# Kernel tuning notes

Measured on AMD Instinct MI355X. Metric: run time of the kernel, lower is better.

Reference implementation:

```python
import jax, jax.numpy as jnp
import numpy as np

B, T, F_IN = 64, 396, 128
D_MODEL, N_HEAD, D_QKV, D_FF = 768, 8, 96, 3072
N_LAYERS, N_OUT, REL_D = 6, 256, 100


def setup_inputs():
    key = jax.random.key(0)
    cnt = [0]
    def rn(shape, std=1.0):
        cnt[0] += 1
        return jax.random.normal(jax.random.fold_in(key, cnt[0]), shape, jnp.float32) * std
    inp = {"x_raw": rn((B, T, F_IN))}
    def add_rb(p, cin, cout):
        inp[p + "_c1_w"] = rn((cout, cin, 3), (2.0 / (cin * 3)) ** 0.5)
        inp[p + "_c1_b"] = rn((cout,), 0.01)
        inp[p + "_bn1_s"] = 1.0 + rn((cout,), 0.1)
        inp[p + "_bn1_b"] = rn((cout,), 0.1)
        inp[p + "_c2_w"] = rn((cout, cout, 3), (2.0 / (cout * 3)) ** 0.5)
        inp[p + "_c2_b"] = rn((cout,), 0.01)
        inp[p + "_bn2_s"] = 1.0 + rn((cout,), 0.1)
        inp[p + "_bn2_b"] = rn((cout,), 0.1)
        inp[p + "_cr_w"] = rn((cout, cin, 1), (2.0 / cin) ** 0.5)
        inp[p + "_cr_b"] = rn((cout,), 0.01)
        inp[p + "_bnr_s"] = 1.0 + rn((cout,), 0.1)
        inp[p + "_bnr_b"] = rn((cout,), 0.1)
    add_rb("rb1", F_IN, D_MODEL)
    add_rb("rb2", D_MODEL, D_MODEL)
    inp["w_in_w"] = rn((D_MODEL, D_MODEL), D_MODEL ** -0.5)
    inp["w_in_b"] = rn((D_MODEL,), 0.01)
    inp["cls_token"] = jnp.zeros((1, 1, D_MODEL), jnp.float32)
    xav = (2.0 / (D_MODEL + D_QKV)) ** 0.5
    inp["wq"] = rn((N_LAYERS, N_HEAD, D_MODEL, D_QKV), xav)
    inp["wk"] = rn((N_LAYERS, N_HEAD, D_MODEL, D_QKV), xav)
    inp["wv"] = rn((N_LAYERS, N_HEAD, D_MODEL, D_QKV), xav)
    inp["wo"] = rn((N_LAYERS, N_HEAD, D_QKV, D_MODEL), xav)
    inp["rel_emb"] = rn((N_LAYERS, N_HEAD, 2 * REL_D + 1, D_QKV), D_QKV ** -0.5)
    inp["ln1_g"] = jnp.ones((N_LAYERS, D_MODEL), jnp.float32)
    inp["ln1_b"] = jnp.zeros((N_LAYERS, D_MODEL), jnp.float32)
    inp["ln2_g"] = jnp.ones((N_LAYERS, D_MODEL), jnp.float32)
    inp["ln2_b"] = jnp.zeros((N_LAYERS, D_MODEL), jnp.float32)
    inp["ff1_w"] = rn((N_LAYERS, D_FF, D_MODEL), (2.0 / D_MODEL) ** 0.5)
    inp["ff1_b"] = rn((N_LAYERS, D_FF), 0.01)
    inp["ff2_w"] = rn((N_LAYERS, D_MODEL, D_FF), (1.0 / D_FF) ** 0.5)
    inp["ff2_b"] = rn((N_LAYERS, D_MODEL), 0.01)
    inp["w_out_w"] = rn((N_OUT, D_MODEL), D_MODEL ** -0.5)
    inp["w_out_b"] = rn((N_OUT,), 0.01)
    return inp


def _conv1d(x, w, b, stride=1):
    # x: [B, Cin, T], w: [Cout, Cin, K]
    pad = (w.shape[-1] - 1) // 2
    y = jax.lax.conv_general_dilated(x, w, (stride,), [(pad, pad)],
                                     dimension_numbers=("NCH", "OIH", "NCH"))
    return y + b[None, :, None]


def _bn(x, s, b):
    # eval-mode BatchNorm1d folded into per-channel affine
    return x * s[None, :, None] + b[None, :, None]


def _resblock(x, c1w, c1b, s1, b1, c2w, c2b, s2, b2, crw, crb, sr, br, stride):
    h = jax.nn.relu(_bn(_conv1d(x, c1w, c1b, stride), s1, b1))
    h = _bn(_conv1d(h, c2w, c2b), s2, b2)
    r = _bn(_conv1d(x, crw, crb, stride), sr, br)
    return jax.nn.relu(h + r)


def _layer_norm(x, g, b, eps=1e-5):
    m = jnp.mean(x, -1, keepdims=True)
    v = jnp.mean((x - m) ** 2, -1, keepdims=True)
    return (x - m) * jax.lax.rsqrt(v + eps) * g + b


def _attention(x, wq, wk, wv, wo, rel):
    # x: [B, L, D]; relative-positional attention (fairseq LearnedRelativePositionalEmbedding, unmasked)
    L = x.shape[1]
    q = jnp.einsum("btf,hfa->bhta", x, wq) * (D_QKV ** -0.5)
    k = jnp.einsum("btf,hfa->bhta", x, wk)
    v = jnp.einsum("btf,hfa->bhta", x, wv)
    logits = jnp.einsum("bhqa,bhka->bhqk", q, k)
    # narrow embeddings to the 2L-1 relative positions used (L <= REL_D)
    start = REL_D - L
    rel_used = rel[:, start:start + 2 * L - 1, :]  # [h, 2L-1, a]
    pos_all = jnp.einsum("bhqa,hma->bhqm", q, rel_used)  # [B,h,L,2L-1]
    idx = jnp.arange(L)[None, :] - jnp.arange(L)[:, None] + (L - 1)  # [L,L], rel->abs skew
    logits = logits + jnp.take_along_axis(pos_all, idx[None, None], axis=3)
    probs = jax.nn.softmax(logits, axis=-1)
    o = jnp.einsum("bhqk,bhka->bhqa", probs, v)
    return jnp.einsum("bhta,haf->btf", o, wo)


def reference(x_raw, rb1_c1_w, rb1_c1_b, rb1_bn1_s, rb1_bn1_b, rb1_c2_w, rb1_c2_b, rb1_bn2_s, rb1_bn2_b, rb1_cr_w, rb1_cr_b, rb1_bnr_s, rb1_bnr_b, rb2_c1_w, rb2_c1_b, rb2_bn1_s, rb2_bn1_b, rb2_c2_w, rb2_c2_b, rb2_bn2_s, rb2_bn2_b, rb2_cr_w, rb2_cr_b, rb2_bnr_s, rb2_bnr_b, w_in_w, w_in_b, cls_token, wq, wk, wv, wo, rel_emb, ln1_g, ln1_b, ln2_g, ln2_b, ff1_w, ff1_b, ff2_w, ff2_b, w_out_w, w_out_b):
    x = jnp.transpose(x_raw, (0, 2, 1))  # [B, F_IN, T]
    x = _resblock(x, rb1_c1_w, rb1_c1_b, rb1_bn1_s, rb1_bn1_b, rb1_c2_w, rb1_c2_b, rb1_bn2_s, rb1_bn2_b, rb1_cr_w, rb1_cr_b, rb1_bnr_s, rb1_bnr_b, 2)
    x = _resblock(x, rb2_c1_w, rb2_c1_b, rb2_bn1_s, rb2_bn1_b, rb2_c2_w, rb2_c2_b, rb2_bn2_s, rb2_bn2_b, rb2_cr_w, rb2_cr_b, rb2_bnr_s, rb2_bnr_b, 2)
    x = jnp.transpose(x, (0, 2, 1))  # [B, T', D]
    x = x @ w_in_w.T + w_in_b
    cls = jnp.broadcast_to(cls_token, (x.shape[0], 1, D_MODEL))
    x = jnp.concatenate([cls, x], axis=1)  # [B, L, D], L = T'+1
    for l in range(N_LAYERS):
        a = _attention(x, wq[l], wk[l], wv[l], wo[l], rel_emb[l])
        x = _layer_norm(x + a, ln1_g[l], ln1_b[l])
        h = jax.nn.relu(x @ ff1_w[l].T + ff1_b[l]) @ ff2_w[l].T + ff2_b[l]
        x = _layer_norm(x + h, ln2_g[l], ln2_b[l])
    return x[:, 0, :] @ w_out_w.T + w_out_b
```

## Files before the change

kernel.cpp:

```cpp
#include <hip/hip_runtime.h>

typedef _Float16 h8 __attribute__((ext_vector_type(8)));
typedef float f4 __attribute__((ext_vector_type(4)));

namespace {

constexpr int DM   = 768;
constexpr int NHEAD= 8;
constexpr int DQ   = 96;
constexpr int DFF  = 3072;
constexpr int NL   = 6;
constexpr int B_   = 64;
constexpr int T0   = 396, T1 = 198, T2 = 99;
constexpr int FIN  = 128;
constexpr int L_   = 100;
constexpr int MSEQ = B_ * L_;
constexpr int M1   = B_ * T1;
constexpr int M2   = B_ * T2;
constexpr int NREL = 201;
constexpr int POSN = 256;
constexpr int RELK = 128;

enum { EPI_F32 = 0, EPI_RELU_H, EPI_H, EPI_CONV_F32, EPI_CONV_RELU_H, EPI_CONV_ADD_RELU_H };

__device__ __forceinline__ void g2l16(const _Float16* g, _Float16* l)
{
    __builtin_amdgcn_global_load_lds(
        (const __attribute__((address_space(1))) unsigned int*)g,
        (__attribute__((address_space(3))) unsigned int*)l,
        16, 0, 0);
}

template<bool CONV, int EPI, bool OPAD, int MI>
__global__ __launch_bounds__(256)
void gemm6_k(const _Float16* __restrict__ A, const _Float16* __restrict__ B,
             float* __restrict__ Cf, _Float16* __restrict__ Ch,
             const float* __restrict__ bias, const float* __restrict__ bns,
             const float* __restrict__ bnb, const float* __restrict__ res,
             int M, int N, int K, int lda,
             int T_out, int Tp_in, int stride_t, int KS, int in_off,
             int gx, int gxy,
             size_t a_z, size_t b_z, size_t c_z)
{
    constexpr int TM = MI * 32;
    __shared__ _Float16 As[2][TM * 64];
    __shared__ _Float16 Bs[2][128 * 64];

    const unsigned nwg = gridDim.x, orig = blockIdx.x;
    const unsigned q = nwg >> 3, rr_ = nwg & 7;
    const unsigned xcd = orig & 7, idx = orig >> 3;
    const unsigned wgid = (xcd < rr_) ? xcd * (q + 1) + idx
                                      : rr_ * (q + 1) + (xcd - rr_) * q + idx;
    const int bz  = (int)(wgid / (unsigned)gxy);
    const int rem = (int)(wgid - (unsigned)bz * (unsigned)gxy);
    const int by  = rem / gx;
    const int bx  = rem - by * gx;

    A += (size_t)bz * a_z;
    B += (size_t)bz * b_z;

    const int tid  = threadIdx.x;
    const int lane = tid & 63;
    const int wid  = tid >> 6;
    const int m0   = by * TM;
    const int n0   = bx * 128;
    const int wm   = (wid >> 1) * (MI * 16);
    const int wn   = (wid & 1) * 64;

    f4 acc[MI][4];
    #pragma unroll
    for (int i = 0; i < MI; ++i)
        #pragma unroll
        for (int j = 0; j < 4; ++j)
            #pragma unroll
            for (int p = 0; p < 4; ++p) acc[i][j][p] = 0.0f;

    const int colh = (((lane & 7) ^ ((lane >> 3) & 7)) << 3);
    size_t aoff[MI];
    #pragma unroll
    for (int i = 0; i < MI; ++i) {
        int m = min(m0 + wid * (MI * 8) + i * 8 + (lane >> 3), M - 1);
        if (CONV) {
            int ab = m / T_out, at = m - ab * T_out;
            aoff[i] = ((size_t)ab * Tp_in + at * stride_t + in_off) * lda + colh;
        } else {
            aoff[i] = (size_t)m * lda + colh;
        }
    }
    size_t boff[4];
    #pragma unroll
    for (int i = 0; i < 4; ++i)
        boff[i] = (size_t)(n0 + wid * 32 + i * 8 + (lane >> 3)) * K + colh;
    const size_t bdk = (size_t)N * K;

    const int fr  = lane & 15;
    const int grp = lane >> 4;

    const int ks64 = K >> 6;
    const int NS   = (CONV ? KS : 1) * ks64;

    auto stage = [&](int step, int buf) {
        int dk = 0, kk = step;
        if (CONV) { dk = step / ks64; kk = step - dk * ks64; }
        const int k0  = kk << 6;
        const size_t adk = CONV ? (size_t)dk * lda : 0;
        const size_t bdo = (size_t)dk * bdk;
        #pragma unroll
        for (int i = 0; i < MI; ++i)
            g2l16(A + aoff[i] + adk + k0, &As[buf][(wid * (MI * 8) + i * 8) * 64]);
        #pragma unroll
        for (int i = 0; i < 4; ++i)
            g2l16(B + boff[i] + bdo + k0, &Bs[buf][(wid * 32 + i * 8) * 64]);
    };

    stage(0, 0);
    __syncthreads();

    for (int step = 0; step < NS; ++step) {
        const int cur = step & 1;
        const _Float16* As_ = As[cur];
        const _Float16* Bs_ = Bs[cur];

        const int co0 = ((grp ^ (fr & 7)) << 3);
        h8 af0[MI], bf0[4];
        #pragma unroll
        for (int mi = 0; mi < MI; ++mi)
            af0[mi] = *(const h8*)&As_[(wm + mi * 16 + fr) * 64 + co0];
        #pragma unroll
        for (int ni = 0; ni < 4; ++ni)
            bf0[ni] = *(const h8*)&Bs_[(wn + ni * 16 + fr) * 64 + co0];

        if (step + 1 < NS) stage(step + 1, cur ^ 1);

        #pragma unroll
        for (int mi = 0; mi < MI; ++mi)
            #pragma unroll
            for (int ni = 0; ni < 4; ++ni)
                acc[mi][ni] = __builtin_amdgcn_mfma_f32_16x16x32_f16(
                    af0[mi], bf0[ni], acc[mi][ni], 0, 0, 0);

        const int co1 = (((4 + grp) ^ (fr & 7)) << 3);
        h8 af1[MI], bf1[4];
        #pragma unroll
        for (int mi = 0; mi < MI; ++mi)
            af1[mi] = *(const h8*)&As_[(wm + mi * 16 + fr) * 64 + co1];
        #pragma unroll
        for (int ni = 0; ni < 4; ++ni)
            bf1[ni] = *(const h8*)&Bs_[(wn + ni * 16 + fr) * 64 + co1];
        #pragma unroll
        for (int mi = 0; mi < MI; ++mi)
            #pragma unroll
            for (int ni = 0; ni < 4; ++ni)
                acc[mi][ni] = __builtin_amdgcn_mfma_f32_16x16x32_f16(
                    af1[mi], bf1[ni], acc[mi][ni], 0, 0, 0);

        __syncthreads();
    }

    const int frc = lane & 15;
    const int fq4 = (lane >> 4) * 4;
    float*    Cfo = Cf ? Cf + (size_t)bz * c_z : nullptr;
    _Float16* Cho = Ch ? Ch + (size_t)bz * c_z : nullptr;
    #pragma unroll
    for (int mi = 0; mi < MI; ++mi)
        #pragma unroll
        for (int ni = 0; ni < 4; ++ni)
            #pragma unroll
            for (int r = 0; r < 4; ++r) {
                int row = m0 + wm + mi * 16 + fq4 + r;
                int col = n0 + wn + ni * 16 + frc;
                if (row >= M) continue;
                float v = acc[mi][ni][r];
                size_t roff;
                if (OPAD) {
                    int ab = row / T_out, at = row - ab * T_out;
                    roff = ((size_t)ab * (T_out + 2) + at + 1) * N + col;
                } else {
                    roff = (size_t)row * N + col;
                }
                if (EPI == EPI_F32) {
                    if (bias) v += bias[col];
                    Cfo[roff] = v;
                } else if (EPI == EPI_RELU_H) {
                    if (bias) v += bias[col];
                    Cho[roff] = (_Float16)fmaxf(v, 0.0f);
                } else if (EPI == EPI_H) {
                    Cho[roff] = (_Float16)v;
                } else if (EPI == EPI_CONV_F32) {
                    v = bns[col] * (v + bias[col]) + bnb[col];
                    Cfo[roff] = v;
                } else if (EPI == EPI_CONV_RELU_H) {
                    v = bns[col] * (v + bias[col]) + bnb[col];
                    Cho[roff] = (_Float16)fmaxf(v, 0.0f);
                } else {
                    v = bns[col] * (v + bias[col]) + bnb[col] + res[(size_t)row * N + col];
                    Cho[roff] = (_Float16)fmaxf(v, 0.0f);
                }
            }
}


__global__ void f2h_k(const float* __restrict__ in, _Float16* __restrict__ out,
                      long n, float scale)
{
    long i = (long)blockIdx.x * blockDim.x + threadIdx.x;
    if (i < n) out[i] = (_Float16)(in[i] * scale);
}

__global__ void f2h_pad_k(const float* __restrict__ in, _Float16* __restrict__ out)
{
    long i = (long)blockIdx.x * blockDim.x + threadIdx.x;
    if (i >= (long)B_ * 398 * FIN) return;
    int  c = (int)(i % FIN);
    long r = i / FIN;
    int  t = (int)(r % 398);
    int  b = (int)(r / 398);
    float v = (t == 0 || t == 397) ? 0.0f
            : in[((long)b * T0 + (t - 1)) * FIN + c];
    out[i] = (_Float16)v;
}

__global__ void zero_pad_k(_Float16* __restrict__ buf, int Tp, int C)
{
    long i = (long)blockIdx.x * blockDim.x + threadIdx.x;
    if (i >= (long)B_ * 2 * C) return;
    int  c = (int)(i % C);
    long r = i / C;
    int  hi = (int)(r % 2);
    int  b  = (int)(r / 2);
    buf[((size_t)b * Tp + (hi ? Tp - 1 : 0)) * C + c] = (_Float16)0.0f;
}

__global__ void pack_qkv_k(const float* __restrict__ wq, const float* __restrict__ wk,
                           const float* __restrict__ wv, _Float16* __restrict__ out)
{
    long i = (long)blockIdx.x * blockDim.x + threadIdx.x;
    if (i >= (long)NL * 2304 * DM) return;
    int  f = (int)(i % DM);
    long r = i / DM;
    int  n = (int)(r % 2304);
    int  l = (int)(r / 2304);
    int  s = n / DM, hn = n % DM, h = hn / DQ, a = hn % DQ;
    const float* src = (s == 0) ? wq : ((s == 1) ? wk : wv);
    out[i] = (_Float16)src[(((long)l * NHEAD + h) * DM + f) * DQ + a];
}

__global__ void pack_wo_k(const float* __restrict__ wo, _Float16* __restrict__ out)
{
    long i = (long)blockIdx.x * blockDim.x + threadIdx.x;
    if (i >= (long)NL * DM * DM) return;
    int  ha = (int)(i % DM);
    long r  = i / DM;
    int  f  = (int)(r % DM);
    int  l  = (int)(r / DM);
    int  h = ha / DQ, a = ha % DQ;
    out[i] = (_Float16)wo[(((long)l * NHEAD + h) * DQ + a) * DM + f];
}

__global__ void pack_conv_k(const float* __restrict__ w, _Float16* __restrict__ out,
                            int Cout, int Cin, int KS)
{
    long i = (long)blockIdx.x * blockDim.x + threadIdx.x;
    if (i >= (long)Cout * Cin * KS) return;
    int  ci = (int)(i % Cin);
    long r  = i / Cin;
    int  co = (int)(r % Cout);
    int  dk = (int)(r / Cout);
    out[i] = (_Float16)w[((long)co * Cin + ci) * KS + dk];
}

__global__ void pack_rel_k(const float* __restrict__ rel, _Float16* __restrict__ out)
{
    long i = (long)blockIdx.x * blockDim.x + threadIdx.x;
    if (i >= (long)NL * NHEAD * POSN * RELK) return;
    int  k = (int)(i & (RELK - 1));
    long r = i >> 7;
    int  n = (int)(r & (POSN - 1));
    long r2 = r >> 8;
    int  h = (int)(r2 & (NHEAD - 1));
    int  l = (int)(r2 >> 3);
    float v = 0.0f;
    if (n < NREL && k < DQ)
        v = rel[(((long)l * NHEAD + h) * NREL + n) * DQ + k] * 0.10206207261596575f;
    out[i] = (_Float16)v;
}

__global__ void concat_k(const float* __restrict__ xlin, const float* __restrict__ cls,
                         float* __restrict__ xf, _Float16* __restrict__ xh)
{
    long i = (long)blockIdx.x * blockDim.x + threadIdx.x;
    if (i >= (long)MSEQ * DM) return;
    int  c = (int)(i % DM);
    long m = i / DM;
    int  b = (int)(m / L_), t = (int)(m % L_);
    float v = (t == 0) ? cls[c] : xlin[((long)b * (L_ - 1) + (t - 1)) * DM + c];
    xf[i] = v;
    xh[i] = (_Float16)v;
}

__global__ __launch_bounds__(256)
void ln_k(const float* x, const float* __restrict__ d,
          const float* __restrict__ g, const float* __restrict__ bb,
          float* xo, _Float16* __restrict__ xh)
{
    long row = blockIdx.x;
    const float* xr = x + row * DM;
    const float* dr = d + row * DM;
    float v[3];
    float s = 0.0f;
    #pragma unroll
    for (int k = 0; k < 3; ++k) {
        int c = threadIdx.x + 256 * k;
        v[k] = xr[c] + dr[c];
        s += v[k];
    }
    __shared__ float red[8];
    #pragma unroll
    for (int o = 32; o; o >>= 1) s += __shfl_xor(s, o, 64);
    int w = threadIdx.x >> 6, lane = threadIdx.x & 63;
    if (lane == 0) red[w] = s;
    __syncthreads();
    s = red[0] + red[1] + red[2] + red[3];
    float mean = s * (1.0f / DM);
    float vs = 0.0f;
    #pragma unroll
    for (int k = 0; k < 3; ++k) { float t = v[k] - mean; vs += t * t; }
    #pragma unroll
    for (int o = 32; o; o >>= 1) vs += __shfl_xor(vs, o, 64);
    if (lane == 0) red[4 + w] = vs;
    __syncthreads();
    vs = red[4] + red[5] + red[6] + red[7];
    float rstd = rsqrtf(vs * (1.0f / DM) + 1e-5f);
    #pragma unroll
    for (int k = 0; k < 3; ++k) {
        int c = threadIdx.x + 256 * k;
        float y = (v[k] - mean) * rstd * g[c] + bb[c];
        xo[row * DM + c] = y;
        xh[row * DM + c] = (_Float16)y;
    }
}

constexpr int LP = 128;
constexpr int KP = 104;
constexpr int PP = 136;

__global__ __launch_bounds__(256)
void attn_k(const _Float16* __restrict__ qkv, const _Float16* __restrict__ pos,
            _Float16* __restrict__ o)
{
    __shared__ __align__(16) char smem[60928];
    _Float16* Ks = (_Float16*)smem;
    _Float16* Ps = (_Float16*)smem;
    _Float16* Vt = (_Float16*)(smem + 34816);

    const int h = blockIdx.x, b = blockIdx.y;
    const int tid = threadIdx.x, lane = tid & 63, w = tid >> 6;
    const _Float16* base = qkv + (size_t)b * L_ * 2304 + h * DQ;
    const float qscale = 0.10206207261596575f;

    {
        int row = tid >> 1;
        int c0  = (tid & 1) * 48;
        const bool real = row < L_;
        const _Float16* krow = base + 768 + (size_t)row * 2304;
        #pragma unroll
        for (int q = 0; q < 6; ++q) {
            int c = c0 + q * 8;
            h8 kv;
            #pragma unroll
            for (int e = 0; e < 8; ++e) kv[e] = (_Float16)0.0f;
            if (real) kv = *(const h8*)(krow + c);
            *(h8*)&Ks[row * KP + c] = kv;
        }
        for (int idx = tid; idx < DQ * LP; idx += 256) {
            int a = idx % DQ, j = idx / DQ;
            _Float16 v = (_Float16)0.0f;
            if (j < L_) v = base[1536 + (size_t)j * 2304 + a];
            Vt[a * PP + j] = v;
        }
    }
    __syncthreads();

    const int fr = lane & 15;
    const int fk = (lane >> 4) * 8;
    const int rbase = w * 32 + ((lane >> 4) << 2);

    f4 acc[2][8];
    #pragma unroll
    for (int mi = 0; mi < 2; ++mi)
        #pragma unroll
        for (int ni = 0; ni < 8; ++ni)
            #pragma unroll
            for (int q = 0; q < 4; ++q) acc[mi][ni][q] = 0.0f;

    #pragma unroll
    for (int k0 = 0; k0 < DQ; k0 += 32) {
        h8 a0 = *(const h8*)(base + (size_t)(w * 32 + fr) * 2304 + k0 + fk);
        h8 a1 = *(const h8*)(base + (size_t)(w * 32 + 16 + fr) * 2304 + k0 + fk);
        #pragma unroll
        for (int ni = 0; ni < 8; ++ni) {
            h8 bv = *(const h8*)&Ks[(ni * 16 + fr) * KP + k0 + fk];
            acc[0][ni] = __builtin_amdgcn_mfma_f32_16x16x32_f16(a0, bv, acc[0][ni], 0, 0, 0);
            acc[1][ni] = __builtin_amdgcn_mfma_f32_16x16x32_f16(a1, bv, acc[1][ni], 0, 0, 0);
        }
    }

    const _Float16* posb = pos + ((size_t)h * MSEQ + (size_t)b * L_) * POSN;
    #pragma unroll
    for (int mi = 0; mi < 2; ++mi)
        #pragma unroll
        for (int r = 0; r < 4; ++r) {
            int i = rbase + mi * 16 + r;
            float s[8];
            #pragma unroll
            for (int ni = 0; ni < 8; ++ni) {
                int j = ni * 16 + fr;
                float v = -3.0e38f;
                if (i < L_ && j < L_)
                    v = acc[mi][ni][r] * qscale
                      + (float)posb[(size_t)i * POSN + (j - i + (L_ - 1))];
                s[ni] = v;
            }
            float m = s[0];
            #pragma unroll
            for (int ni = 1; ni < 8; ++ni) m = fmaxf(m, s[ni]);
            #pragma unroll
            for (int msk = 1; msk < 16; msk <<= 1) m = fmaxf(m, __shfl_xor(m, msk, 64));
            float sum = 0.0f;
            #pragma unroll
            for (int ni = 0; ni < 8; ++ni) { s[ni] = __expf(s[ni] - m); sum += s[ni]; }
            #pragma unroll
            for (int msk = 1; msk < 16; msk <<= 1) sum += __shfl_xor(sum, msk, 64);
            float inv = 1.0f / sum;
            #pragma unroll
            for (int ni = 0; ni < 8; ++ni) acc[mi][ni][r] = s[ni] * inv;
        }

    __syncthreads();

    #pragma unroll
    for (int mi = 0; mi < 2; ++mi)
        #pragma unroll
        for (int r = 0; r < 4; ++r) {
            int i = rbase + mi * 16 + r;
            #pragma unroll
            for (int ni = 0; ni < 8; ++ni)
                Ps[i * PP + ni * 16 + fr] = (_Float16)acc[mi][ni][r];
        }
    __syncthreads();

    f4 acc2[2][6];
    #pragma unroll
    for (int mi = 0; mi < 2; ++mi)
        #pragma unroll
        for (int ni = 0; ni < 6; ++ni)
            #pragma unroll
            for (int q = 0; q < 4; ++q) acc2[mi][ni][q] = 0.0f;

    #pragma unroll
    for (int k0 = 0; k0 < LP; k0 += 32) {
        h8 a0 = *(const h8*)&Ps[(w * 32 + fr) * PP + k0 + fk];
        h8 a1 = *(const h8*)&Ps[(w * 32 + 16 + fr) * PP + k0 + fk];
        #pragma unroll
        for (int ni = 0; ni < 6; ++ni) {
            h8 bv = *(const h8*)&Vt[(ni * 16 + fr) * PP + k0 + fk];
            acc2[0][ni] = __builtin_amdgcn_mfma_f32_16x16x32_f16(a0, bv, acc2[0][ni], 0, 0, 0);
            acc2[1][ni] = __builtin_amdgcn_mfma_f32_16x16x32_f16(a1, bv, acc2[1][ni], 0, 0, 0);
        }
    }

    _Float16* ob = o + (size_t)b * L_ * DM + h * DQ;
    #pragma unroll
    for (int mi = 0; mi < 2; ++mi)
        #pragma unroll
        for (int r = 0; r < 4; ++r) {
            int i = rbase + mi * 16 + r;
            if (i < L_) {
                #pragma unroll
                for (int ni = 0; ni < 6; ++ni)
                    ob[(size_t)i * DM + ni * 16 + fr] = (_Float16)acc2[mi][ni][r];
            }
        }
}

__global__ __launch_bounds__(256)
void out_k(const float* __restrict__ xseq, const float* __restrict__ w,
           const float* __restrict__ bias, float* __restrict__ out)
{
    __shared__ float xs[DM];
    int b = blockIdx.x;
    for (int c = threadIdx.x; c < DM; c += 256) xs[c] = xseq[(size_t)b * L_ * DM + c];
    __syncthreads();
    int n = threadIdx.x;
    const f4* wr = (const f4*)(w + (size_t)n * DM);
    float acc = 0.0f;
    #pragma unroll 4
    for (int k4 = 0; k4 < DM / 4; ++k4) {
        f4 wv = wr[k4];
        f4 xv = *(const f4*)&xs[k4 * 4];
        acc += wv[0]*xv[0] + wv[1]*xv[1] + wv[2]*xv[2] + wv[3]*xv[3];
    }
    out[(size_t)b * 256 + n] = acc + bias[n];
}

}

extern "C" void kernel_launch(void* const* d_in, const int* in_sizes, int n_in,
                              void* d_out, int out_size, void* d_ws, size_t ws_size,
                              hipStream_t stream)
{
    (void)in_sizes; (void)n_in; (void)out_size; (void)ws_size;

    const float* x_raw   = (const float*)d_in[0];
    const float* rb1_c1w = (const float*)d_in[1];
    const float* rb1_c1b = (const float*)d_in[2];
    const float* rb1_s1  = (const float*)d_in[3];
    const float* rb1_b1  = (const float*)d_in[4];
    const float* rb1_c2w = (const float*)d_in[5];
    const float* rb1_c2b = (const float*)d_in[6];
    const float* rb1_s2  = (const float*)d_in[7];
    const float* rb1_b2  = (const float*)d_in[8];
    const float* rb1_crw = (const float*)d_in[9];
    const float* rb1_crb = (const float*)d_in[10];
    const float* rb1_sr  = (const float*)d_in[11];
    const float* rb1_br  = (const float*)d_in[12];
    const float* rb2_c1w = (const float*)d_in[13];
    const float* rb2_c1b = (const float*)d_in[14];
    const float* rb2_s1  = (const float*)d_in[15];
    const float* rb2_b1  = (const float*)d_in[16];
    const float* rb2_c2w = (const float*)d_in[17];
    const float* rb2_c2b = (const float*)d_in[18];
    const float* rb2_s2  = (const float*)d_in[19];
    const float* rb2_b2  = (const float*)d_in[20];
    const float* rb2_crw = (const float*)d_in[21];
    const float* rb2_crb = (const float*)d_in[22];
    const float* rb2_sr  = (const float*)d_in[23];
    const float* rb2_br  = (const float*)d_in[24];
    const float* w_in_w  = (const float*)d_in[25];
    const float* w_in_b  = (const float*)d_in[26];
    const float* cls     = (const float*)d_in[27];
    const float* wq      = (const float*)d_in[28];
    const float* wk      = (const float*)d_in[29];
    const float* wv      = (const float*)d_in[30];
    const float* wo      = (const float*)d_in[31];
    const float* rel     = (const float*)d_in[32];
    const float* ln1g    = (const float*)d_in[33];
    const float* ln1b    = (const float*)d_in[34];
    const float* ln2g    = (const float*)d_in[35];
    const float* ln2b    = (const float*)d_in[36];
    const float* ff1w    = (const float*)d_in[37];
    const float* ff1b    = (const float*)d_in[38];
    const float* ff2w    = (const float*)d_in[39];
    const float* ff2b    = (const float*)d_in[40];
    const float* w_out_w = (const float*)d_in[41];
    const float* w_out_b = (const float*)d_in[42];

    char* base = (char*)d_ws;
    size_t off = 0;
    auto carve = [&](size_t bytes) -> char* {
        char* p = base + off;
        off = (off + bytes + 255) & ~(size_t)255;
        return p;
    };
    _Float16* w_in_h = (_Float16*)carve((size_t)589824 * 2);
    _Float16* qkvw   = (_Float16*)carve((size_t)10616832 * 2);
    _Float16* wow    = (_Float16*)carve((size_t)3538944 * 2);
    _Float16* ff1h   = (_Float16*)carve((size_t)14155776 * 2);
    _Float16* ff2h   = (_Float16*)carve((size_t)14155776 * 2);
    _Float16* relh   = (_Float16*)carve((size_t)NL * NHEAD * POSN * RELK * 2);
    _Float16* cw11   = (_Float16*)carve((size_t)294912 * 2);
    _Float16* cw12   = (_Float16*)carve((size_t)1769472 * 2);
    _Float16* cw1r   = (_Float16*)carve((size_t)98304 * 2);
    _Float16* cw21   = (_Float16*)carve((size_t)1769472 * 2);
    _Float16* cw22   = (_Float16*)carve((size_t)1769472 * 2);
    _Float16* cw2r   = (_Float16*)carve((size_t)589824 * 2);
    _Float16* xrawp  = (_Float16*)carve((size_t)B_ * 398 * FIN * 2);
    float*    xseq_f = (float*)carve((size_t)4915200 * 4);
    _Float16* xseq_h = (_Float16*)carve((size_t)4915200 * 2);
    _Float16* qkvb   = (_Float16*)carve((size_t)14745600 * 2);
    _Float16* ohb    = (_Float16*)carve((size_t)4915200 * 2);
    float*    af     = (float*)carve((size_t)4915200 * 4);
    char*     hhreg  = carve((size_t)19660800 * 2);
    float*    yf     = (float*)carve((size_t)4915200 * 4);
    _Float16* h1_rb1 = qkvb;
    float*    r_rb1  = (float*)hhreg;
    _Float16* out1   = (_Float16*)af;
    _Float16* h1_rb2 = (_Float16*)xseq_f;
    float*    r_rb2  = yf;
    _Float16* out2   = ohb;
    float*    xlin   = (float*)hhreg;
    _Float16* posh   = (_Float16*)hhreg;
    _Float16* ffh    = (_Float16*)hhreg;

    dim3 blk(256, 1, 1);
    auto grd = [](long n) { return dim3((unsigned)((n + 255) / 256), 1, 1); };
    #define NWG(M, N, TM, GZ) dim3((unsigned)(((N) / 128) * (((M) + (TM) - 1) / (TM)) * (GZ)), 1, 1)
    #define GXY(M, N, TM) ((N) / 128), (((N) / 128) * (((M) + (TM) - 1) / (TM)))

    f2h_pad_k<<<grd((long)B_ * 398 * FIN), blk, 0, stream>>>(x_raw, xrawp);
    zero_pad_k<<<grd((long)B_ * 2 * DM), blk, 0, stream>>>(h1_rb1, 200, DM);
    zero_pad_k<<<grd((long)B_ * 2 * DM), blk, 0, stream>>>(out1, 200, DM);
    zero_pad_k<<<grd((long)B_ * 2 * DM), blk, 0, stream>>>(h1_rb2, 101, DM);
    f2h_k<<<grd(589824), blk, 0, stream>>>(w_in_w, w_in_h, 589824, 1.0f);
    f2h_k<<<grd(14155776), blk, 0, stream>>>(ff1w, ff1h, 14155776, 1.0f);
    f2h_k<<<grd(14155776), blk, 0, stream>>>(ff2w, ff2h, 14155776, 1.0f);
    pack_rel_k<<<grd((long)NL * NHEAD * POSN * RELK), blk, 0, stream>>>(rel, relh);
    pack_qkv_k<<<grd((long)NL * 2304 * DM), blk, 0, stream>>>(wq, wk, wv, qkvw);
    pack_wo_k<<<grd((long)NL * DM * DM), blk, 0, stream>>>(wo, wow);
    pack_conv_k<<<grd(294912), blk, 0, stream>>>(rb1_c1w, cw11, DM, FIN, 3);
    pack_conv_k<<<grd(1769472), blk, 0, stream>>>(rb1_c2w, cw12, DM, DM, 3);
    pack_conv_k<<<grd(98304), blk, 0, stream>>>(rb1_crw, cw1r, DM, FIN, 1);
    pack_conv_k<<<grd(1769472), blk, 0, stream>>>(rb2_c1w, cw21, DM, DM, 3);
    pack_conv_k<<<grd(1769472), blk, 0, stream>>>(rb2_c2w, cw22, DM, DM, 3);
    pack_conv_k<<<grd(589824), blk, 0, stream>>>(rb2_crw, cw2r, DM, DM, 1);

    gemm6_k<true, EPI_CONV_F32, false, 4><<<NWG(M1, DM, 128, 1), blk, 0, stream>>>(
        xrawp, cw1r, r_rb1, nullptr, rb1_crb, rb1_sr, rb1_br, nullptr,
        M1, DM, FIN, FIN, T1, 398, 2, 1, 1, GXY(M1, DM, 128), 0, 0, 0);
    gemm6_k<true, EPI_CONV_RELU_H, true, 4><<<NWG(M1, DM, 128, 1), blk, 0, stream>>>(
        xrawp, cw11, nullptr, h1_rb1, rb1_c1b, rb1_s1, rb1_b1, nullptr,
        M1, DM, FIN, FIN, T1, 398, 2, 3, 0, GXY(M1, DM, 128), 0, 0, 0);
    gemm6_k<true, EPI_CONV_ADD_RELU_H, true, 4><<<NWG(M1, DM, 128, 1), blk, 0, stream>>>(
        h1_rb1, cw12, nullptr, out1, rb1_c2b, rb1_s2, rb1_b2, r_rb1,
        M1, DM, DM, DM, T1, 200, 1, 3, 0, GXY(M1, DM, 128), 0, 0, 0);

    gemm6_k<true, EPI_CONV_F32, false, 2><<<NWG(M2, DM, 64, 1), blk, 0, stream>>>(
        out1, cw2r, r_rb2, nullptr, rb2_crb, rb2_sr, rb2_br, nullptr,
        M2, DM, DM, DM, T2, 200, 2, 1, 1, GXY(M2, DM, 64), 0, 0, 0);
    gemm6_k<true, EPI_CONV_RELU_H, true, 2><<<NWG(M2, DM, 64, 1), blk, 0, stream>>>(
        out1, cw21, nullptr, h1_rb2, rb2_c1b, rb2_s1, rb2_b1, nullptr,
        M2, DM, DM, DM, T2, 200, 2, 3, 0, GXY(M2, DM, 64), 0, 0, 0);
    gemm6_k<true, EPI_CONV_ADD_RELU_H, false, 2><<<NWG(M2, DM, 64, 1), blk, 0, stream>>>(
        h1_rb2, cw22, nullptr, out2, rb2_c2b, rb2_s2, rb2_b2, r_rb2,
        M2, DM, DM, DM, T2, 101, 1, 3, 0, GXY(M2, DM, 64), 0, 0, 0);

    gemm6_k<false, EPI_F32, false, 2><<<NWG(M2, DM, 64, 1), blk, 0, stream>>>(
        out2, w_in_h, xlin, nullptr, w_in_b, nullptr, nullptr, nullptr,
        M2, DM, DM, DM, 0, 0, 0, 0, 0, GXY(M2, DM, 64), 0, 0, 0);
    concat_k<<<grd((long)MSEQ * DM), blk, 0, stream>>>(xlin, cls, xseq_f, xseq_h);

    for (int l = 0; l < NL; ++l) {
        gemm6_k<false, EPI_H, false, 4><<<NWG(MSEQ, 2304, 128, 1), blk, 0, stream>>>(
            xseq_h, qkvw + (size_t)l * 2304 * DM, nullptr, qkvb,
            nullptr, nullptr, nullptr, nullptr,
            MSEQ, 2304, DM, DM, 0, 0, 0, 0, 0, GXY(MSEQ, 2304, 128), 0, 0, 0);
        gemm6_k<false, EPI_H, false, 4><<<NWG(MSEQ, POSN, 128, NHEAD), blk, 0, stream>>>(
            qkvb, relh + (size_t)l * NHEAD * POSN * RELK, nullptr, posh,
            nullptr, nullptr, nullptr, nullptr,
            MSEQ, POSN, RELK, 2304, 0, 0, 0, 0, 0, GXY(MSEQ, POSN, 128),
            (size_t)DQ, (size_t)POSN * RELK, (size_t)MSEQ * POSN);
        attn_k<<<dim3(NHEAD, B_, 1), blk, 0, stream>>>(qkvb, posh, ohb);
        gemm6_k<false, EPI_F32, false, 2><<<NWG(MSEQ, DM, 64, 1), blk, 0, stream>>>(
            ohb, wow + (size_t)l * DM * DM, af, nullptr,
            nullptr, nullptr, nullptr, nullptr,
            MSEQ, DM, DM, DM, 0, 0, 0, 0, 0, GXY(MSEQ, DM, 64), 0, 0, 0);
        ln_k<<<dim3(MSEQ), blk, 0, stream>>>(xseq_f, af, ln1g + l * DM, ln1b + l * DM,
                                             xseq_f, xseq_h);
        gemm6_k<false, EPI_RELU_H, false, 4><<<NWG(MSEQ, DFF, 128, 1), blk, 0, stream>>>(
            xseq_h, ff1h + (size_t)l * DFF * DM, nullptr, ffh,
            ff1b + l * DFF, nullptr, nullptr, nullptr,
            MSEQ, DFF, DM, DM, 0, 0, 0, 0, 0, GXY(MSEQ, DFF, 128), 0, 0, 0);
        gemm6_k<false, EPI_F32, false, 2><<<NWG(MSEQ, DM, 64, 1), blk, 0, stream>>>(
            ffh, ff2h + (size_t)l * DM * DFF, yf, nullptr,
            ff2b + l * DM, nullptr, nullptr, nullptr,
            MSEQ, DM, DFF, DFF, 0, 0, 0, 0, 0, GXY(MSEQ, DM, 64), 0, 0, 0);
        ln_k<<<dim3(MSEQ), blk, 0, stream>>>(xseq_f, yf, ln2g + l * DM, ln2b + l * DM,
                                             xseq_f, xseq_h);
    }

    out_k<<<dim3(B_), blk, 0, stream>>>(xseq_f, w_out_w, w_out_b, (float*)d_out);
    #undef NWG
    #undef GXY
}
```

Measured before the change: 2.024 ms.

## Split conv GEMM into single-buffered kernel, store residual in fp16, vectorize weight casts

The conv GEMMs move into a separate single-buffered kernel (gemm5_k) with a nested tap/K loop, so the integer division per step is gone. The non-conv gemm6_k is trimmed of its conv parameters. The residual branch of both resblocks is now stored as fp16 instead of fp32, which halves its write and read traffic. Weight fp32-to-fp16 conversions use an 8-wide vectorized kernel. Removing double buffering from the conv path may expose global load latency, and the fp16 residual adds rounding error.

```diff
diff --git a/kernel.cpp b/kernel.cpp
--- a/kernel.cpp
+++ b/kernel.cpp
@@ -21,7 +21,7 @@
 constexpr int POSN = 256;
 constexpr int RELK = 128;
 
-enum { EPI_F32 = 0, EPI_RELU_H, EPI_H, EPI_CONV_F32, EPI_CONV_RELU_H, EPI_CONV_ADD_RELU_H };
+enum { EPI_F32 = 0, EPI_RELU_H, EPI_H, EPI_CONV_BN_H, EPI_CONV_RELU_H, EPI_CONV_ADD_RELU_H };
 
 __device__ __forceinline__ void g2l16(const _Float16* g, _Float16* l)
 {
@@ -31,132 +31,13 @@
         16, 0, 0);
 }
 
-template<bool CONV, int EPI, bool OPAD, int MI>
-__global__ __launch_bounds__(256)
-void gemm6_k(const _Float16* __restrict__ A, const _Float16* __restrict__ B,
-             float* __restrict__ Cf, _Float16* __restrict__ Ch,
-             const float* __restrict__ bias, const float* __restrict__ bns,
-             const float* __restrict__ bnb, const float* __restrict__ res,
-             int M, int N, int K, int lda,
-             int T_out, int Tp_in, int stride_t, int KS, int in_off,
-             int gx, int gxy,
-             size_t a_z, size_t b_z, size_t c_z)
-{
-    constexpr int TM = MI * 32;
-    __shared__ _Float16 As[2][TM * 64];
-    __shared__ _Float16 Bs[2][128 * 64];
-
-    const unsigned nwg = gridDim.x, orig = blockIdx.x;
-    const unsigned q = nwg >> 3, rr_ = nwg & 7;
-    const unsigned xcd = orig & 7, idx = orig >> 3;
-    const unsigned wgid = (xcd < rr_) ? xcd * (q + 1) + idx
-                                      : rr_ * (q + 1) + (xcd - rr_) * q + idx;
-    const int bz  = (int)(wgid / (unsigned)gxy);
-    const int rem = (int)(wgid - (unsigned)bz * (unsigned)gxy);
-    const int by  = rem / gx;
-    const int bx  = rem - by * gx;
-
-    A += (size_t)bz * a_z;
-    B += (size_t)bz * b_z;
-
-    const int tid  = threadIdx.x;
-    const int lane = tid & 63;
-    const int wid  = tid >> 6;
-    const int m0   = by * TM;
-    const int n0   = bx * 128;
-    const int wm   = (wid >> 1) * (MI * 16);
-    const int wn   = (wid & 1) * 64;
-
-    f4 acc[MI][4];
-    #pragma unroll
-    for (int i = 0; i < MI; ++i)
-        #pragma unroll
-        for (int j = 0; j < 4; ++j)
-            #pragma unroll
-            for (int p = 0; p < 4; ++p) acc[i][j][p] = 0.0f;
-
-    const int colh = (((lane & 7) ^ ((lane >> 3) & 7)) << 3);
-    size_t aoff[MI];
-    #pragma unroll
-    for (int i = 0; i < MI; ++i) {
-        int m = min(m0 + wid * (MI * 8) + i * 8 + (lane >> 3), M - 1);
-        if (CONV) {
-            int ab = m / T_out, at = m - ab * T_out;
-            aoff[i] = ((size_t)ab * Tp_in + at * stride_t + in_off) * lda + colh;
-        } else {
-            aoff[i] = (size_t)m * lda + colh;
-        }
-    }
-    size_t boff[4];
-    #pragma unroll
-    for (int i = 0; i < 4; ++i)
-        boff[i] = (size_t)(n0 + wid * 32 + i * 8 + (lane >> 3)) * K + colh;
-    const size_t bdk = (size_t)N * K;
-
-    const int fr  = lane & 15;
-    const int grp = lane >> 4;
-
-    const int ks64 = K >> 6;
-    const int NS   = (CONV ? KS : 1) * ks64;
-
-    auto stage = [&](int step, int buf) {
-        int dk = 0, kk = step;
-        if (CONV) { dk = step / ks64; kk = step - dk * ks64; }
-        const int k0  = kk << 6;
-        const size_t adk = CONV ? (size_t)dk * lda : 0;
-        const size_t bdo = (size_t)dk * bdk;
-        #pragma unroll
-        for (int i = 0; i < MI; ++i)
-            g2l16(A + aoff[i] + adk + k0, &As[buf][(wid * (MI * 8) + i * 8) * 64]);
-        #pragma unroll
-        for (int i = 0; i < 4; ++i)
-            g2l16(B + boff[i] + bdo + k0, &Bs[buf][(wid * 32 + i * 8) * 64]);
-    };
-
-    stage(0, 0);
-    __syncthreads();
-
-    for (int step = 0; step < NS; ++step) {
-        const int cur = step & 1;
-        const _Float16* As_ = As[cur];
-        const _Float16* Bs_ = Bs[cur];
-
-        const int co0 = ((grp ^ (fr & 7)) << 3);
-        h8 af0[MI], bf0[4];
-        #pragma unroll
-        for (int mi = 0; mi < MI; ++mi)
-            af0[mi] = *(const h8*)&As_[(wm + mi * 16 + fr) * 64 + co0];
-        #pragma unroll
-        for (int ni = 0; ni < 4; ++ni)
-            bf0[ni] = *(const h8*)&Bs_[(wn + ni * 16 + fr) * 64 + co0];
-
-        if (step + 1 < NS) stage(step + 1, cur ^ 1);
-
-        #pragma unroll
-        for (int mi = 0; mi < MI; ++mi)
-            #pragma unroll
-            for (int ni = 0; ni < 4; ++ni)
-                acc[mi][ni] = __builtin_amdgcn_mfma_f32_16x16x32_f16(
-                    af0[mi], bf0[ni], acc[mi][ni], 0, 0, 0);
-
-        const int co1 = (((4 + grp) ^ (fr & 7)) << 3);
-        h8 af1[MI], bf1[4];
-        #pragma unroll
-        for (int mi = 0; mi < MI; ++mi)
-            af1[mi] = *(const h8*)&As_[(wm + mi * 16 + fr) * 64 + co1];
-        #pragma unroll
-        for (int ni = 0; ni < 4; ++ni)
-            bf1[ni] = *(const h8*)&Bs_[(wn + ni * 16 + fr) * 64 + co1];
-        #pragma unroll
-        for (int mi = 0; mi < MI; ++mi)
-            #pragma unroll
-            for (int ni = 0; ni < 4; ++ni)
-                acc[mi][ni] = __builtin_amdgcn_mfma_f32_16x16x32_f16(
-                    af1[mi], bf1[ni], acc[mi][ni], 0, 0, 0);
-
-        __syncthreads();
-    }
-
+template<int EPI, bool OPAD, int MI>
+__device__ __forceinline__ void epilogue(
+    f4 (&acc)[MI][4], int lane, int m0, int wm, int n0, int wn,
+    int M, int N, int T_out, int bz,
+    float* Cf, _Float16* Ch, const float* bias, const float* bns,
+    const float* bnb, const _Float16* res, size_t c_z)
+{
     const int frc = lane & 15;
     const int fq4 = (lane >> 4) * 4;
     float*    Cfo = Cf ? Cf + (size_t)bz * c_z : nullptr;
@@ -186,25 +67,249 @@
                     Cho[roff] = (_Float16)fmaxf(v, 0.0f);
                 } else if (EPI == EPI_H) {
                     Cho[roff] = (_Float16)v;
-                } else if (EPI == EPI_CONV_F32) {
+                } else if (EPI == EPI_CONV_BN_H) {
                     v = bns[col] * (v + bias[col]) + bnb[col];
-                    Cfo[roff] = v;
+                    Cho[roff] = (_Float16)v;
                 } else if (EPI == EPI_CONV_RELU_H) {
                     v = bns[col] * (v + bias[col]) + bnb[col];
                     Cho[roff] = (_Float16)fmaxf(v, 0.0f);
                 } else {
-                    v = bns[col] * (v + bias[col]) + bnb[col] + res[(size_t)row * N + col];
+                    v = bns[col] * (v + bias[col]) + bnb[col]
+                      + (float)res[(size_t)row * N + col];
                     Cho[roff] = (_Float16)fmaxf(v, 0.0f);
                 }
             }
 }
 
+template<int EPI, bool OPAD, int MI>
+__global__ __launch_bounds__(256)
+void gemm5_k(const _Float16* __restrict__ A, const _Float16* __restrict__ B,
+             float* __restrict__ Cf, _Float16* __restrict__ Ch,
+             const float* __restrict__ bias, const float* __restrict__ bns,
+             const float* __restrict__ bnb, const _Float16* __restrict__ res,
+             int M, int N, int K, int lda,
+             int T_out, int Tp_in, int stride_t, int KS, int in_off,
+             int gx, int gxy)
+{
+    constexpr int TM = MI * 32;
+    __shared__ _Float16 As[TM * 64];
+    __shared__ _Float16 Bs[128 * 64];
+
+    const unsigned nwg = gridDim.x, orig = blockIdx.x;
+    const unsigned q = nwg >> 3, rr_ = nwg & 7;
+    const unsigned xcd = orig & 7, idx = orig >> 3;
+    const unsigned wgid = (xcd < rr_) ? xcd * (q + 1) + idx
+                                      : rr_ * (q + 1) + (xcd - rr_) * q + idx;
+    const int by  = (int)(wgid / (unsigned)gx);
+    const int bx  = (int)(wgid - (unsigned)by * (unsigned)gx);
+    (void)gxy;
+
+    const int tid  = threadIdx.x;
+    const int lane = tid & 63;
+    const int wid  = tid >> 6;
+    const int m0   = by * TM;
+    const int n0   = bx * 128;
+    const int wm   = (wid >> 1) * (MI * 16);
+    const int wn   = (wid & 1) * 64;
+
+    f4 acc[MI][4];
+    #pragma unroll
+    for (int i = 0; i < MI; ++i)
+        #pragma unroll
+        for (int j = 0; j < 4; ++j)
+            #pragma unroll
+            for (int p = 0; p < 4; ++p) acc[i][j][p] = 0.0f;
+
+    const int colh = (((lane & 7) ^ ((lane >> 3) & 7)) << 3);
+    size_t aoff[MI];
+    #pragma unroll
+    for (int i = 0; i < MI; ++i) {
+        int m = min(m0 + wid * (MI * 8) + i * 8 + (lane >> 3), M - 1);
+        int ab = m / T_out, at = m - ab * T_out;
+        aoff[i] = ((size_t)ab * Tp_in + at * stride_t + in_off) * lda + colh;
+    }
+    size_t boff[4];
+    #pragma unroll
+    for (int i = 0; i < 4; ++i)
+        boff[i] = (size_t)(n0 + wid * 32 + i * 8 + (lane >> 3)) * K + colh;
+    const size_t bdk = (size_t)N * K;
+
+    const int fr  = lane & 15;
+    const int grp = lane >> 4;
+
+    for (int dk = 0; dk < KS; ++dk) {
+        const size_t adk = (size_t)dk * lda;
+        const size_t bdo = (size_t)dk * bdk;
+
+        for (int k0 = 0; k0 < K; k0 += 64) {
+            #pragma unroll
+            for (int i = 0; i < MI; ++i)
+                g2l16(A + aoff[i] + adk + k0, &As[(wid * (MI * 8) + i * 8) * 64]);
+            #pragma unroll
+            for (int i = 0; i < 4; ++i)
+                g2l16(B + boff[i] + bdo + k0, &Bs[(wid * 32 + i * 8) * 64]);
+            __syncthreads();
+
+            #pragma unroll
+            for (int kh = 0; kh < 2; ++kh) {
+                const int co = (((kh * 4 + grp) ^ (fr & 7)) << 3);
+                h8 af[MI], bf[4];
+                #pragma unroll
+                for (int mi = 0; mi < MI; ++mi)
+                    af[mi] = *(const h8*)&As[(wm + mi * 16 + fr) * 64 + co];
+                #pragma unroll
+                for (int ni = 0; ni < 4; ++ni)
+                    bf[ni] = *(const h8*)&Bs[(wn + ni * 16 + fr) * 64 + co];
+                #pragma unroll
+                for (int mi = 0; mi < MI; ++mi)
+                    #pragma unroll
+                    for (int ni = 0; ni < 4; ++ni)
+                        acc[mi][ni] = __builtin_amdgcn_mfma_f32_16x16x32_f16(
+                            af[mi], bf[ni], acc[mi][ni], 0, 0, 0);
+            }
+            __syncthreads();
+        }
+    }
+
+    epilogue<EPI, OPAD, MI>(acc, lane, m0, wm, n0, wn, M, N, T_out, 0,
+                            Cf, Ch, bias, bns, bnb, res, 0);
+}
+
+template<int EPI, int MI>
+__global__ __launch_bounds__(256)
+void gemm6_k(const _Float16* __restrict__ A, const _Float16* __restrict__ B,
+             float* __restrict__ Cf, _Float16* __restrict__ Ch,
+             const float* __restrict__ bias,
+             int M, int N, int K, int lda,
+             int gx, int gxy,
+             size_t a_z, size_t b_z, size_t c_z)
+{
+    constexpr int TM = MI * 32;
+    __shared__ _Float16 As[2][TM * 64];
+    __shared__ _Float16 Bs[2][128 * 64];
+
+    const unsigned nwg = gridDim.x, orig = blockIdx.x;
+    const unsigned q = nwg >> 3, rr_ = nwg & 7;
+    const unsigned xcd = orig & 7, idx = orig >> 3;
+    const unsigned wgid = (xcd < rr_) ? xcd * (q + 1) + idx
+                                      : rr_ * (q + 1) + (xcd - rr_) * q + idx;
+    const int bz  = (int)(wgid / (unsigned)gxy);
+    const int rem = (int)(wgid - (unsigned)bz * (unsigned)gxy);
+    const int by  = rem / gx;
+    const int bx  = rem - by * gx;
+
+    A += (size_t)bz * a_z;
+    B += (size_t)bz * b_z;
+
+    const int tid  = threadIdx.x;
+    const int lane = tid & 63;
+    const int wid  = tid >> 6;
+    const int m0   = by * TM;
+    const int n0   = bx * 128;
+    const int wm   = (wid >> 1) * (MI * 16);
+    const int wn   = (wid & 1) * 64;
+
+    f4 acc[MI][4];
+    #pragma unroll
+    for (int i = 0; i < MI; ++i)
+        #pragma unroll
+        for (int j = 0; j < 4; ++j)
+            #pragma unroll
+            for (int p = 0; p < 4; ++p) acc[i][j][p] = 0.0f;
+
+    const int colh = (((lane & 7) ^ ((lane >> 3) & 7)) << 3);
+    size_t aoff[MI];
+    #pragma unroll
+    for (int i = 0; i < MI; ++i) {
+        int m = min(m0 + wid * (MI * 8) + i * 8 + (lane >> 3), M - 1);
+        aoff[i] = (size_t)m * lda + colh;
+    }
+    size_t boff[4];
+    #pragma unroll
+    for (int i = 0; i < 4; ++i)
+        boff[i] = (size_t)(n0 + wid * 32 + i * 8 + (lane >> 3)) * K + colh;
+
+    const int fr  = lane & 15;
+    const int grp = lane >> 4;
+    const int NS  = K >> 6;
+
+    auto stage = [&](int step, int buf) {
+        const int k0 = step << 6;
+        #pragma unroll
+        for (int i = 0; i < MI; ++i)
+            g2l16(A + aoff[i] + k0, &As[buf][(wid * (MI * 8) + i * 8) * 64]);
+        #pragma unroll
+        for (int i = 0; i < 4; ++i)
+            g2l16(B + boff[i] + k0, &Bs[buf][(wid * 32 + i * 8) * 64]);
+    };
+
+    stage(0, 0);
+    __syncthreads();
+
+    for (int step = 0; step < NS; ++step) {
+        const int cur = step & 1;
+        const _Float16* As_ = As[cur];
+        const _Float16* Bs_ = Bs[cur];
+
+        const int co0 = ((grp ^ (fr & 7)) << 3);
+        h8 af0[MI], bf0[4];
+        #pragma unroll
+        for (int mi = 0; mi < MI; ++mi)
+            af0[mi] = *(const h8*)&As_[(wm + mi * 16 + fr) * 64 + co0];
+        #pragma unroll
+        for (int ni = 0; ni < 4; ++ni)
+            bf0[ni] = *(const h8*)&Bs_[(wn + ni * 16 + fr) * 64 + co0];
+
+        if (step + 1 < NS) stage(step + 1, cur ^ 1);
+
+        #pragma unroll
+        for (int mi = 0; mi < MI; ++mi)
+            #pragma unroll
+            for (int ni = 0; ni < 4; ++ni)
+                acc[mi][ni] = __builtin_amdgcn_mfma_f32_16x16x32_f16(
+                    af0[mi], bf0[ni], acc[mi][ni], 0, 0, 0);
+
+        const int co1 = (((4 + grp) ^ (fr & 7)) << 3);
+        h8 af1[MI], bf1[4];
+        #pragma unroll
+        for (int mi = 0; mi < MI; ++mi)
+            af1[mi] = *(const h8*)&As_[(wm + mi * 16 + fr) * 64 + co1];
+        #pragma unroll
+        for (int ni = 0; ni < 4; ++ni)
+            bf1[ni] = *(const h8*)&Bs_[(wn + ni * 16 + fr) * 64 + co1];
+        #pragma unroll
+        for (int mi = 0; mi < MI; ++mi)
+            #pragma unroll
+            for (int ni = 0; ni < 4; ++ni)
+                acc[mi][ni] = __builtin_amdgcn_mfma_f32_16x16x32_f16(
+                    af1[mi], bf1[ni], acc[mi][ni], 0, 0, 0);
+
+        __syncthreads();
+    }
+
+    epilogue<EPI, false, MI>(acc, lane, m0, wm, n0, wn, M, N, 0, bz,
+                             Cf, Ch, bias, nullptr, nullptr, nullptr, c_z);
+}
+
 
 __global__ void f2h_k(const float* __restrict__ in, _Float16* __restrict__ out,
                       long n, float scale)
 {
     long i = (long)blockIdx.x * blockDim.x + threadIdx.x;
     if (i < n) out[i] = (_Float16)(in[i] * scale);
+}
+
+__global__ void f2h8_k(const float* __restrict__ in, _Float16* __restrict__ out,
+                       long n8)
+{
+    long i = (long)blockIdx.x * blockDim.x + threadIdx.x;
+    if (i >= n8) return;
+    f4 a = ((const f4*)in)[2 * i];
+    f4 b = ((const f4*)in)[2 * i + 1];
+    h8 o;
+    #pragma unroll
+    for (int j = 0; j < 4; ++j) { o[j] = (_Float16)a[j]; o[4 + j] = (_Float16)b[j]; }
+    ((h8*)out)[i] = o;
 }
 
 __global__ void f2h_pad_k(const float* __restrict__ in, _Float16* __restrict__ out)
@@ -583,10 +688,10 @@
     char*     hhreg  = carve((size_t)19660800 * 2);
     float*    yf     = (float*)carve((size_t)4915200 * 4);
     _Float16* h1_rb1 = qkvb;
-    float*    r_rb1  = (float*)hhreg;
+    _Float16* r_rb1h = (_Float16*)hhreg;
     _Float16* out1   = (_Float16*)af;
     _Float16* h1_rb2 = (_Float16*)xseq_f;
-    float*    r_rb2  = yf;
+    _Float16* r_rb2h = (_Float16*)yf;
     _Float16* out2   = ohb;
     float*    xlin   = (float*)hhreg;
     _Float16* posh   = (_Float16*)hhreg;
@@ -601,9 +706,9 @@
     zero_pad_k<<<grd((long)B_ * 2 * DM), blk, 0, stream>>>(h1_rb1, 200, DM);
     zero_pad_k<<<grd((long)B_ * 2 * DM), blk, 0, stream>>>(out1, 200, DM);
     zero_pad_k<<<grd((long)B_ * 2 * DM), blk, 0, stream>>>(h1_rb2, 101, DM);
-    f2h_k<<<grd(589824), blk, 0, stream>>>(w_in_w, w_in_h, 589824, 1.0f);
-    f2h_k<<<grd(14155776), blk, 0, stream>>>(ff1w, ff1h, 14155776, 1.0f);
-    f2h_k<<<grd(14155776), blk, 0, stream>>>(ff2w, ff2h, 14155776, 1.0f);
+    f2h8_k<<<grd(589824 / 8), blk, 0, stream>>>(w_in_w, w_in_h, 589824 / 8);
+    f2h8_k<<<grd(14155776 / 8), blk, 0, stream>>>(ff1w, ff1h, 14155776 / 8);
+    f2h8_k<<<grd(14155776 / 8), blk, 0, stream>>>(ff2w, ff2h, 14155776 / 8);
     pack_rel_k<<<grd((long)NL * NHEAD * POSN * RELK), blk, 0, stream>>>(rel, relh);
     pack_qkv_k<<<grd((long)NL * 2304 * DM), blk, 0, stream>>>(wq, wk, wv, qkvw);
     pack_wo_k<<<grd((long)NL * DM * DM), blk, 0, stream>>>(wo, wow);
@@ -614,56 +719,51 @@
     pack_conv_k<<<grd(1769472), blk, 0, stream>>>(rb2_c2w, cw22, DM, DM, 3);
     pack_conv_k<<<grd(589824), blk, 0, stream>>>(rb2_crw, cw2r, DM, DM, 1);
 
-    gemm6_k<true, EPI_CONV_F32, false, 4><<<NWG(M1, DM, 128, 1), blk, 0, stream>>>(
-        xrawp, cw1r, r_rb1, nullptr, rb1_crb, rb1_sr, rb1_br, nullptr,
-        M1, DM, FIN, FIN, T1, 398, 2, 1, 1, GXY(M1, DM, 128), 0, 0, 0);
-    gemm6_k<true, EPI_CONV_RELU_H, true, 4><<<NWG(M1, DM, 128, 1), blk, 0, stream>>>(
+    gemm5_k<EPI_CONV_BN_H, false, 4><<<NWG(M1, DM, 128, 1), blk, 0, stream>>>(
+        xrawp, cw1r, nullptr, r_rb1h, rb1_crb, rb1_sr, rb1_br, nullptr,
+        M1, DM, FIN, FIN, T1, 398, 2, 1, 1, GXY(M1, DM, 128));
+    gemm5_k<EPI_CONV_RELU_H, true, 4><<<NWG(M1, DM, 128, 1), blk, 0, stream>>>(
         xrawp, cw11, nullptr, h1_rb1, rb1_c1b, rb1_s1, rb1_b1, nullptr,
-        M1, DM, FIN, FIN, T1, 398, 2, 3, 0, GXY(M1, DM, 128), 0, 0, 0);
-    gemm6_k<true, EPI_CONV_ADD_RELU_H, true, 4><<<NWG(M1, DM, 128, 1), blk, 0, stream>>>(
-        h1_rb1, cw12, nullptr, out1, rb1_c2b, rb1_s2, rb1_b2, r_rb1,
-        M1, DM, DM, DM, T1, 200, 1, 3, 0, GXY(M1, DM, 128), 0, 0, 0);
-
-    gemm6_k<true, EPI_CONV_F32, false, 2><<<NWG(M2, DM, 64, 1), blk, 0, stream>>>(
-        out1, cw2r, r_rb2, nullptr, rb2_crb, rb2_sr, rb2_br, nullptr,
-        M2, DM, DM, DM, T2, 200, 2, 1, 1, GXY(M2, DM, 64), 0, 0, 0);
-    gemm6_k<true, EPI_CONV_RELU_H, true, 2><<<NWG(M2, DM, 64, 1), blk, 0, stream>>>(
+        M1, DM, FIN, FIN, T1, 398, 2, 3, 0, GXY(M1, DM, 128));
+    gemm5_k<EPI_CONV_ADD_RELU_H, true, 4><<<NWG(M1, DM, 128, 1), blk, 0, stream>>>(
+        h1_rb1, cw12, nullptr, out1, rb1_c2b, rb1_s2, rb1_b2, r_rb1h,
+        M1, DM, DM, DM, T1, 200, 1, 3, 0, GXY(M1, DM, 128));
+
+    gemm5_k<EPI_CONV_BN_H, false, 2><<<NWG(M2, DM, 64, 1), blk, 0, stream>>>(
+        out1, cw2r, nullptr, r_rb2h, rb2_crb, rb2_sr, rb2_br, nullptr,
+        M2, DM, DM, DM, T2, 200, 2, 1, 1, GXY(M2, DM, 64));
+    gemm5_k<EPI_CONV_RELU_H, true, 2><<<NWG(M2, DM, 64, 1), blk, 0, stream>>>(
         out1, cw21, nullptr, h1_rb2, rb2_c1b, rb2_s1, rb2_b1, nullptr,
-        M2, DM, DM, DM, T2, 200, 2, 3, 0, GXY(M2, DM, 64), 0, 0, 0);
-    gemm6_k<true, EPI_CONV_ADD_RELU_H, false, 2><<<NWG(M2, DM, 64, 1), blk, 0, stream>>>(
-        h1_rb2, cw22, nullptr, out2, rb2_c2b, rb2_s2, rb2_b2, r_rb2,
-        M2, DM, DM, DM, T2, 101, 1, 3, 0, GXY(M2, DM, 64), 0, 0, 0);
-
-    gemm6_k<false, EPI_F32, false, 2><<<NWG(M2, DM, 64, 1), blk, 0, stream>>>(
-        out2, w_in_h, xlin, nullptr, w_in_b, nullptr, nullptr, nullptr,
-        M2, DM, DM, DM, 0, 0, 0, 0, 0, GXY(M2, DM, 64), 0, 0, 0);
+        M2, DM, DM, DM, T2, 200, 2, 3, 0, GXY(M2, DM, 64));
+    gemm5_k<EPI_CONV_ADD_RELU_H, false, 2><<<NWG(M2, DM, 64, 1), blk, 0, stream>>>(
+        h1_rb2, cw22, nullptr, out2, rb2_c2b, rb2_s2, rb2_b2, r_rb2h,
+        M2, DM, DM, DM, T2, 101, 1, 3, 0, GXY(M2, DM, 64));
+
+    gemm6_k<EPI_F32, 2><<<NWG(M2, DM, 64, 1), blk, 0, stream>>>(
+        out2, w_in_h, xlin, nullptr, w_in_b,
+        M2, DM, DM, DM, GXY(M2, DM, 64), 0, 0, 0);
     concat_k<<<grd((long)MSEQ * DM), blk, 0, stream>>>(xlin, cls, xseq_f, xseq_h);
 
     for (int l = 0; l < NL; ++l) {
-        gemm6_k<false, EPI_H, false, 4><<<NWG(MSEQ, 2304, 128, 1), blk, 0, stream>>>(
-            xseq_h, qkvw + (size_t)l * 2304 * DM, nullptr, qkvb,
-            nullptr, nullptr, nullptr, nullptr,
-            MSEQ, 2304, DM, DM, 0, 0, 0, 0, 0, GXY(MSEQ, 2304, 128), 0, 0, 0);
-        gemm6_k<false, EPI_H, false, 4><<<NWG(MSEQ, POSN, 128, NHEAD), blk, 0, stream>>>(
-            qkvb, relh + (size_t)l * NHEAD * POSN * RELK, nullptr, posh,
-            nullptr, nullptr, nullptr, nullptr,
-            MSEQ, POSN, RELK, 2304, 0, 0, 0, 0, 0, GXY(MSEQ, POSN, 128),
+        gemm6_k<EPI_H, 4><<<NWG(MSEQ, 2304, 128, 1), blk, 0, stream>>>(
+            xseq_h, qkvw + (size_t)l * 2304 * DM, nullptr, qkvb, nullptr,
+            MSEQ, 2304, DM, DM, GXY(MSEQ, 2304, 128), 0, 0, 0);
+        gemm6_k<EPI_H, 4><<<NWG(MSEQ, POSN, 128, NHEAD), blk, 0, stream>>>(
+            qkvb, relh + (size_t)l * NHEAD * POSN * RELK, nullptr, posh, nullptr,
+            MSEQ, POSN, RELK, 2304, GXY(MSEQ, POSN, 128),
             (size_t)DQ, (size_t)POSN * RELK, (size_t)MSEQ * POSN);
         attn_k<<<dim3(NHEAD, B_, 1), blk, 0, stream>>>(qkvb, posh, ohb);
-        gemm6_k<false, EPI_F32, false, 2><<<NWG(MSEQ, DM, 64, 1), blk, 0, stream>>>(
-            ohb, wow + (size_t)l * DM * DM, af, nullptr,
-            nullptr, nullptr, nullptr, nullptr,
-            MSEQ, DM, DM, DM, 0, 0, 0, 0, 0, GXY(MSEQ, DM, 64), 0, 0, 0);
+        gemm6_k<EPI_F32, 2><<<NWG(MSEQ, DM, 64, 1), blk, 0, stream>>>(
+            ohb, wow + (size_t)l * DM * DM, af, nullptr, nullptr,
+            MSEQ, DM, DM, DM, GXY(MSEQ, DM, 64), 0, 0, 0);
         ln_k<<<dim3(MSEQ), blk, 0, stream>>>(xseq_f, af, ln1g + l * DM, ln1b + l * DM,
                                              xseq_f, xseq_h);
-        gemm6_k<false, EPI_RELU_H, false, 4><<<NWG(MSEQ, DFF, 128, 1), blk, 0, stream>>>(
-            xseq_h, ff1h + (size_t)l * DFF * DM, nullptr, ffh,
-            ff1b + l * DFF, nullptr, nullptr, nullptr,
-            MSEQ, DFF, DM, DM, 0, 0, 0, 0, 0, GXY(MSEQ, DFF, 128), 0, 0, 0);
-        gemm6_k<false, EPI_F32, false, 2><<<NWG(MSEQ, DM, 64, 1), blk, 0, stream>>>(
-            ffh, ff2h + (size_t)l * DM * DFF, yf, nullptr,
-            ff2b + l * DM, nullptr, nullptr, nullptr,
-            MSEQ, DM, DFF, DFF, 0, 0, 0, 0, 0, GXY(MSEQ, DM, 64), 0, 0, 0);
+        gemm6_k<EPI_RELU_H, 4><<<NWG(MSEQ, DFF, 128, 1), blk, 0, stream>>>(
+            xseq_h, ff1h + (size_t)l * DFF * DM, nullptr, ffh, ff1b + l * DFF,
+            MSEQ, DFF, DM, DM, GXY(MSEQ, DFF, 128), 0, 0, 0);
+        gemm6_k<EPI_F32, 2><<<NWG(MSEQ, DM, 64, 1), blk, 0, stream>>>(
+            ffh, ff2h + (size_t)l * DM * DFF, yf, nullptr, ff2b + l * DM,
+            MSEQ, DM, DFF, DFF, GXY(MSEQ, DM, 64), 0, 0, 0);
         ln_k<<<dim3(MSEQ), blk, 0, stream>>>(xseq_f, yf, ln2g + l * DM, ln2b + l * DM,
                                              xseq_f, xseq_h);
     }
```

Result: faster. 1.943 ms, median of 2 (-4.0%).
